# Performance work log

Measured on AMD Instinct MI355X. Metric: run time of the kernel, lower is better.

## Reference

```python
import jax, jax.numpy as jnp
import numpy as np

B, C, H, W = 4, 256, 64, 64

def _conv1x1(x, w, b):
    # x: (B,C,H,W), w: (O,C), b: (O,)  -> (B,O,H,W)
    return jnp.einsum('oc,bchw->bohw', w, x) + b[None, :, None, None]

def setup_inputs() -> dict:
    key = jax.random.key(0)
    ks = jax.random.split(key, 8)
    s = 1.0 / np.sqrt(C)  # conv weight init scale
    return {
        'tgt': jax.random.normal(ks[0], (B, C, H, W), jnp.float32),
        'src': jax.random.normal(ks[1], (B, C, H, W), jnp.float32),
        'q_w': jax.random.normal(ks[2], (C, C), jnp.float32) * s,
        'q_b': jnp.zeros((C,), jnp.float32),
        'k_w': jax.random.normal(ks[3], (C, C), jnp.float32) * s,
        'k_b': jnp.zeros((C,), jnp.float32),
        'v_w': jax.random.normal(ks[4], (C, C), jnp.float32) * s,
        'v_b': jnp.zeros((C,), jnp.float32),
    }

def reference(tgt, src, q_w, q_b, k_w, k_b, v_w, v_b):
    # NOTE: tgt.shape == src.shape here, so the interpolate branch is skipped.
    b, c, h, w = src.shape
    # Faithful to torch: .view(B, -1, C) is a RAW reshape of (B,O,H,W)
    # channel-first memory, NOT a transpose to (B, HW, C) token layout.
    query = _conv1x1(tgt, q_w, q_b).reshape(b, -1, c)  # (B, N, C), N = O*H*W/C = H*W
    key   = _conv1x1(src, k_w, k_b).reshape(b, -1, c)
    value = _conv1x1(src, v_w, v_b).reshape(b, -1, c)
    attn = jnp.einsum('bnc,bmc->bnm', query, key)       # (B, N, N) - materialized as in source
    attn = jax.nn.softmax(attn, axis=-1)
    out = jnp.einsum('bnm,bmc->bnc', attn, value)       # (B, N, C)
    return out.reshape(b, c, h, w)
```

## Files before the change

### kernel.cpp

```cpp
#include <hip/hip_runtime.h>
#include <cmath>

#define B_ 4
#define C_ 256
#define P_ 4096
#define N_ 4096

typedef __bf16 bf16x8 __attribute__((ext_vector_type(8)));
typedef __bf16 bf16x4 __attribute__((ext_vector_type(4)));
typedef float  f32x4  __attribute__((ext_vector_type(4)));

__global__ __launch_bounds__(256) void proj_kernel(
    const float* __restrict__ X, const float* __restrict__ W,
    const float* __restrict__ bias,
    __bf16* __restrict__ Yh, __bf16* __restrict__ Yl)
{
    const int p0 = blockIdx.x * 64;
    const int o0 = blockIdx.y * 64;
    const int b  = blockIdx.z;

    const float* Xb = X + (size_t)b * C_ * P_;
    const size_t ybase = (size_t)b * C_ * P_;

    __shared__ float WsT[32][68];
    __shared__ float Xs[32][64];

    const int tid = threadIdx.x;
    const int tx = tid & 15, ty = tid >> 4;

    float acc[4][4] = {};

    for (int kk = 0; kk < C_; kk += 32) {
        __syncthreads();
        #pragma unroll
        for (int i = 0; i < 8; ++i) {
            int flat = tid + i * 256;
            int r = flat >> 5, c = flat & 31;
            WsT[c][r] = W[(o0 + r) * C_ + (kk + c)];
        }
        #pragma unroll
        for (int i = 0; i < 8; ++i) {
            int flat = tid + i * 256;
            int r = flat >> 6, c = flat & 63;
            Xs[r][c] = Xb[(size_t)(kk + r) * P_ + (p0 + c)];
        }
        __syncthreads();
        #pragma unroll
        for (int k = 0; k < 32; ++k) {
            float4 a4 = *(const float4*)&WsT[k][ty * 4];
            float4 x4 = *(const float4*)&Xs[k][tx * 4];
            const float av[4] = {a4.x, a4.y, a4.z, a4.w};
            const float xv[4] = {x4.x, x4.y, x4.z, x4.w};
            #pragma unroll
            for (int i = 0; i < 4; ++i)
                #pragma unroll
                for (int j = 0; j < 4; ++j)
                    acc[i][j] += av[i] * xv[j];
        }
    }

    #pragma unroll
    for (int i = 0; i < 4; ++i) {
        float bv = bias[o0 + ty * 4 + i];
        bf16x4 h, l;
        #pragma unroll
        for (int j = 0; j < 4; ++j) {
            float y  = acc[i][j] + bv;
            __bf16 hh = (__bf16)y;
            __bf16 ll = (__bf16)(y - (float)hh);
            h[j] = hh; l[j] = ll;
        }
        size_t off = ybase + (size_t)(o0 + ty * 4 + i) * P_ + p0 + tx * 4;
        *(bf16x4*)&Yh[off] = h;
        *(bf16x4*)&Yl[off] = l;
    }
}

__global__ __launch_bounds__(256) void transpose_kernel(
    const ushort* __restrict__ Src, ushort* __restrict__ Dst)
{
    const int n0 = blockIdx.x * 64;
    const int c0 = blockIdx.y * 64;
    const int b  = blockIdx.z;

    const ushort* src = Src + (size_t)b * N_ * C_;
    ushort*       dst = Dst + (size_t)b * N_ * C_;

    __shared__ ushort T[64][65];
    const int tid = threadIdx.x;

    #pragma unroll
    for (int it = 0; it < 4; ++it) {
        int e = tid + it * 256;
        int r = e >> 4, c4 = (e & 15) * 4;
        *(ushort4*)&T[r][c4] = *(const ushort4*)&src[(size_t)(n0 + r) * C_ + c0 + c4];
    }
    __syncthreads();
    #pragma unroll
    for (int it = 0; it < 4; ++it) {
        int e = tid + it * 256;
        int cr = e >> 4, nl = (e & 15) * 4;
        ushort4 v;
        v.x = T[nl + 0][cr]; v.y = T[nl + 1][cr];
        v.z = T[nl + 2][cr]; v.w = T[nl + 3][cr];
        *(ushort4*)&dst[(size_t)(c0 + cr) * N_ + n0 + nl] = v;
    }
}

__global__ __launch_bounds__(256, 1) void attn_kernel(
    const __bf16* __restrict__ Qh, const __bf16* __restrict__ Ql,
    const __bf16* __restrict__ Kh, const __bf16* __restrict__ Kl,
    const __bf16* __restrict__ Vth,
    float* __restrict__ O)
{
    const int b  = blockIdx.y;
    const int n0 = blockIdx.x * 64;
    const size_t base = (size_t)b * N_ * C_;

    const int tid  = threadIdx.x;
    const int w    = tid >> 6;
    const int lane = tid & 63;
    const int l15  = lane & 15;
    const int lg   = lane >> 4;
    const int hsw  = l15 & 7;

    __shared__ __align__(16) __bf16 Ksh[2][64][256];
    __shared__ __align__(16) __bf16 Vsh[256][64];
    __shared__ __align__(16) __bf16 Pl[4][2][16][72];

    const __bf16* qh_p = Qh + base + (size_t)(n0 + w * 16 + l15) * C_ + lg * 8;
    const __bf16* ql_p = Ql + base + (size_t)(n0 + w * 16 + l15) * C_ + lg * 8;
    bf16x8 qfh[8], qfl[8];
    #pragma unroll
    for (int k = 0; k < 8; ++k) {
        qfh[k] = *(const bf16x8*)(qh_p + k * 32);
        qfl[k] = *(const bf16x8*)(ql_p + k * 32);
    }

    f32x4 oc[16];
    #pragma unroll
    for (int c = 0; c < 16; ++c) oc[c] = (f32x4){0.f, 0.f, 0.f, 0.f};
    float m_run[4] = {-1e30f, -1e30f, -1e30f, -1e30f};
    float l_run[4] = {0.f, 0.f, 0.f, 0.f};

    bf16x8 krH[8], krL[8], vrH[8];

    #pragma unroll
    for (int i = 0; i < 8; ++i) {
        int f = i * 256 + tid;
        int r = f >> 5, s = f & 31;
        krH[i] = *(const bf16x8*)(Kh + base + (size_t)(0 + r) * C_ + s * 8);
        krL[i] = *(const bf16x8*)(Kl + base + (size_t)(0 + r) * C_ + s * 8);
        int c = f >> 3, sv = f & 7;
        vrH[i] = *(const bf16x8*)(Vth + base + (size_t)c * N_ + 0 + sv * 8);
    }

    for (int mt = 0; mt < N_; mt += 64) {
        __syncthreads();

        #pragma unroll
        for (int i = 0; i < 8; ++i) {
            int f = i * 256 + tid;
            int r = f >> 5, s = f & 31;
            *(bf16x8*)&Ksh[0][r][(s ^ (r & 7)) * 8] = krH[i];
            *(bf16x8*)&Ksh[1][r][(s ^ (r & 7)) * 8] = krL[i];
            int c = f >> 3, sv = f & 7;
            *(bf16x8*)&Vsh[c][(sv ^ (c & 7)) * 8] = vrH[i];
        }
        __syncthreads();

        if (mt + 64 < N_) {
            const int nmt = mt + 64;
            #pragma unroll
            for (int i = 0; i < 8; ++i) {
                int f = i * 256 + tid;
                int r = f >> 5, s = f & 31;
                krH[i] = *(const bf16x8*)(Kh + base + (size_t)(nmt + r) * C_ + s * 8);
                krL[i] = *(const bf16x8*)(Kl + base + (size_t)(nmt + r) * C_ + s * 8);
                int c = f >> 3, sv = f & 7;
                vrH[i] = *(const bf16x8*)(Vth + base + (size_t)c * N_ + nmt + sv * 8);
            }
        }

        f32x4 sacc[4];
        #pragma unroll
        for (int js = 0; js < 4; ++js) sacc[js] = (f32x4){0.f, 0.f, 0.f, 0.f};

        #pragma unroll
        for (int kk = 0; kk < 8; ++kk) {
            #pragma unroll
            for (int js = 0; js < 4; ++js) {
                bf16x8 kfh = *(const bf16x8*)&Ksh[0][js * 16 + l15][((kk * 4 + lg) ^ hsw) * 8];
                bf16x8 kfl = *(const bf16x8*)&Ksh[1][js * 16 + l15][((kk * 4 + lg) ^ hsw) * 8];
                sacc[js] = __builtin_amdgcn_mfma_f32_16x16x32_bf16(qfh[kk], kfh, sacc[js], 0, 0, 0);
                sacc[js] = __builtin_amdgcn_mfma_f32_16x16x32_bf16(qfh[kk], kfl, sacc[js], 0, 0, 0);
                sacc[js] = __builtin_amdgcn_mfma_f32_16x16x32_bf16(qfl[kk], kfh, sacc[js], 0, 0, 0);
            }
        }

        #pragma unroll
        for (int r = 0; r < 4; ++r) {
            float mx = fmaxf(fmaxf(sacc[0][r], sacc[1][r]), fmaxf(sacc[2][r], sacc[3][r]));
            #pragma unroll
            for (int d = 1; d < 16; d <<= 1)
                mx = fmaxf(mx, __shfl_xor(mx, d, 64));
            if (mx > m_run[r]) {
                float scale = __expf(m_run[r] - mx);
                l_run[r] *= scale;
                #pragma unroll
                for (int c = 0; c < 16; ++c) oc[c][r] *= scale;
                m_run[r] = mx;
            }
            float ss = 0.f;
            #pragma unroll
            for (int js = 0; js < 4; ++js) {
                float pv = __expf(sacc[js][r] - m_run[r]);
                sacc[js][r] = pv;
                ss += pv;
            }
            #pragma unroll
            for (int d = 1; d < 16; d <<= 1)
                ss += __shfl_xor(ss, d, 64);
            l_run[r] += ss;
        }

        #pragma unroll
        for (int js = 0; js < 4; ++js)
            #pragma unroll
            for (int r = 0; r < 4; ++r) {
                float pv = sacc[js][r];
                __bf16 hh = (__bf16)pv;
                __bf16 ll = (__bf16)(pv - (float)hh);
                Pl[w][0][lg * 4 + r][js * 16 + l15] = hh;
                Pl[w][1][lg * 4 + r][js * 16 + l15] = ll;
            }

        bf16x8 pah0 = *(const bf16x8*)&Pl[w][0][l15][lg * 8];
        bf16x8 pah1 = *(const bf16x8*)&Pl[w][0][l15][32 + lg * 8];
        bf16x8 pal0 = *(const bf16x8*)&Pl[w][1][l15][lg * 8];
        bf16x8 pal1 = *(const bf16x8*)&Pl[w][1][l15][32 + lg * 8];

        #pragma unroll
        for (int cs = 0; cs < 16; ++cs) {
            bf16x8 vh0 = *(const bf16x8*)&Vsh[cs * 16 + l15][(lg ^ hsw) * 8];
            bf16x8 vh1 = *(const bf16x8*)&Vsh[cs * 16 + l15][((lg + 4) ^ hsw) * 8];
            f32x4 a = oc[cs];
            a = __builtin_amdgcn_mfma_f32_16x16x32_bf16(pah0, vh0, a, 0, 0, 0);
            a = __builtin_amdgcn_mfma_f32_16x16x32_bf16(pal0, vh0, a, 0, 0, 0);
            a = __builtin_amdgcn_mfma_f32_16x16x32_bf16(pah1, vh1, a, 0, 0, 0);
            a = __builtin_amdgcn_mfma_f32_16x16x32_bf16(pal1, vh1, a, 0, 0, 0);
            oc[cs] = a;
        }
    }

    float inv[4];
    #pragma unroll
    for (int r = 0; r < 4; ++r) inv[r] = 1.0f / l_run[r];
    #pragma unroll
    for (int cs = 0; cs < 16; ++cs)
        #pragma unroll
        for (int r = 0; r < 4; ++r)
            O[base + (size_t)(n0 + w * 16 + lg * 4 + r) * C_ + cs * 16 + l15] =
                oc[cs][r] * inv[r];
}

extern "C" void kernel_launch(void* const* d_in, const int* in_sizes, int n_in,
                              void* d_out, int out_size, void* d_ws, size_t ws_size,
                              hipStream_t stream)
{
    const float* tgt = (const float*)d_in[0];
    const float* src = (const float*)d_in[1];
    const float* qw  = (const float*)d_in[2];
    const float* qb  = (const float*)d_in[3];
    const float* kw  = (const float*)d_in[4];
    const float* kb  = (const float*)d_in[5];
    const float* vw  = (const float*)d_in[6];
    const float* vb  = (const float*)d_in[7];
    float* out = (float*)d_out;

    const size_t SZ = (size_t)B_ * N_ * C_;
    __bf16* w0 = (__bf16*)d_ws;
    __bf16* w1 = w0 + SZ;
    __bf16* w2 = w1 + SZ;
    __bf16* w3 = w2 + SZ;
    __bf16* w4 = w3 + SZ;

    dim3 pgrid(P_ / 64, C_ / 64, B_);
    proj_kernel<<<pgrid, 256, 0, stream>>>(src, vw, vb, w0, w1);
    dim3 tgrid(N_ / 64, C_ / 64, B_);
    transpose_kernel<<<tgrid, 256, 0, stream>>>((const ushort*)w0, (ushort*)w4);
    proj_kernel<<<pgrid, 256, 0, stream>>>(tgt, qw, qb, w0, w1);
    proj_kernel<<<pgrid, 256, 0, stream>>>(src, kw, kb, w2, w3);
    dim3 agrid(N_ / 64, B_);
    attn_kernel<<<agrid, 256, 0, stream>>>(w0, w1, w2, w3, w4, out);
}
```

Measured before the change: 557.7 us.

## Halve KV tile to 32 rows and target two blocks per CU

```diff
diff --git a/kernel.cpp b/kernel.cpp
--- a/kernel.cpp
+++ b/kernel.cpp
@@ -5,6 +5,7 @@
 #define C_ 256
 #define P_ 4096
 #define N_ 4096
+#define KVBLK 32
 
 typedef __bf16 bf16x8 __attribute__((ext_vector_type(8)));
 typedef __bf16 bf16x4 __attribute__((ext_vector_type(4)));
@@ -107,7 +108,7 @@
     }
 }
 
-__global__ __launch_bounds__(256, 1) void attn_kernel(
+__global__ __launch_bounds__(256, 2) void attn_kernel(
     const __bf16* __restrict__ Qh, const __bf16* __restrict__ Ql,
     const __bf16* __restrict__ Kh, const __bf16* __restrict__ Kl,
     const __bf16* __restrict__ Vth,
@@ -124,9 +125,9 @@
     const int lg   = lane >> 4;
     const int hsw  = l15 & 7;
 
-    __shared__ __align__(16) __bf16 Ksh[2][64][256];
-    __shared__ __align__(16) __bf16 Vsh[256][64];
-    __shared__ __align__(16) __bf16 Pl[4][2][16][72];
+    __shared__ __align__(16) __bf16 Ksh[2][KVBLK][256];
+    __shared__ __align__(16) __bf16 Vsh[256][40];
+    __shared__ __align__(16) __bf16 Pl[4][2][16][40];
 
     const __bf16* qh_p = Qh + base + (size_t)(n0 + w * 16 + l15) * C_ + lg * 8;
     const __bf16* ql_p = Ql + base + (size_t)(n0 + w * 16 + l15) * C_ + lg * 8;
@@ -143,53 +144,53 @@
     float m_run[4] = {-1e30f, -1e30f, -1e30f, -1e30f};
     float l_run[4] = {0.f, 0.f, 0.f, 0.f};
 
-    bf16x8 krH[8], krL[8], vrH[8];
-
-    #pragma unroll
-    for (int i = 0; i < 8; ++i) {
+    bf16x8 krH[4], krL[4], vrH[4];
+
+    #pragma unroll
+    for (int i = 0; i < 4; ++i) {
         int f = i * 256 + tid;
         int r = f >> 5, s = f & 31;
-        krH[i] = *(const bf16x8*)(Kh + base + (size_t)(0 + r) * C_ + s * 8);
-        krL[i] = *(const bf16x8*)(Kl + base + (size_t)(0 + r) * C_ + s * 8);
-        int c = f >> 3, sv = f & 7;
-        vrH[i] = *(const bf16x8*)(Vth + base + (size_t)c * N_ + 0 + sv * 8);
-    }
-
-    for (int mt = 0; mt < N_; mt += 64) {
-        __syncthreads();
-
-        #pragma unroll
-        for (int i = 0; i < 8; ++i) {
+        krH[i] = *(const bf16x8*)(Kh + base + (size_t)r * C_ + s * 8);
+        krL[i] = *(const bf16x8*)(Kl + base + (size_t)r * C_ + s * 8);
+        int c = f >> 2, sv = f & 3;
+        vrH[i] = *(const bf16x8*)(Vth + base + (size_t)c * N_ + sv * 8);
+    }
+
+    for (int mt = 0; mt < N_; mt += KVBLK) {
+        __syncthreads();
+
+        #pragma unroll
+        for (int i = 0; i < 4; ++i) {
             int f = i * 256 + tid;
             int r = f >> 5, s = f & 31;
             *(bf16x8*)&Ksh[0][r][(s ^ (r & 7)) * 8] = krH[i];
             *(bf16x8*)&Ksh[1][r][(s ^ (r & 7)) * 8] = krL[i];
-            int c = f >> 3, sv = f & 7;
-            *(bf16x8*)&Vsh[c][(sv ^ (c & 7)) * 8] = vrH[i];
-        }
-        __syncthreads();
-
-        if (mt + 64 < N_) {
-            const int nmt = mt + 64;
-            #pragma unroll
-            for (int i = 0; i < 8; ++i) {
+            int c = f >> 2, sv = f & 3;
+            *(bf16x8*)&Vsh[c][sv * 8] = vrH[i];
+        }
+        __syncthreads();
+
+        if (mt + KVBLK < N_) {
+            const int nmt = mt + KVBLK;
+            #pragma unroll
+            for (int i = 0; i < 4; ++i) {
                 int f = i * 256 + tid;
                 int r = f >> 5, s = f & 31;
                 krH[i] = *(const bf16x8*)(Kh + base + (size_t)(nmt + r) * C_ + s * 8);
                 krL[i] = *(const bf16x8*)(Kl + base + (size_t)(nmt + r) * C_ + s * 8);
-                int c = f >> 3, sv = f & 7;
+                int c = f >> 2, sv = f & 3;
                 vrH[i] = *(const bf16x8*)(Vth + base + (size_t)c * N_ + nmt + sv * 8);
             }
         }
 
-        f32x4 sacc[4];
-        #pragma unroll
-        for (int js = 0; js < 4; ++js) sacc[js] = (f32x4){0.f, 0.f, 0.f, 0.f};
+        f32x4 sacc[2];
+        #pragma unroll
+        for (int js = 0; js < 2; ++js) sacc[js] = (f32x4){0.f, 0.f, 0.f, 0.f};
 
         #pragma unroll
         for (int kk = 0; kk < 8; ++kk) {
             #pragma unroll
-            for (int js = 0; js < 4; ++js) {
+            for (int js = 0; js < 2; ++js) {
                 bf16x8 kfh = *(const bf16x8*)&Ksh[0][js * 16 + l15][((kk * 4 + lg) ^ hsw) * 8];
                 bf16x8 kfl = *(const bf16x8*)&Ksh[1][js * 16 + l15][((kk * 4 + lg) ^ hsw) * 8];
                 sacc[js] = __builtin_amdgcn_mfma_f32_16x16x32_bf16(qfh[kk], kfh, sacc[js], 0, 0, 0);
@@ -200,7 +201,7 @@
 
         #pragma unroll
         for (int r = 0; r < 4; ++r) {
-            float mx = fmaxf(fmaxf(sacc[0][r], sacc[1][r]), fmaxf(sacc[2][r], sacc[3][r]));
+            float mx = fmaxf(sacc[0][r], sacc[1][r]);
             #pragma unroll
             for (int d = 1; d < 16; d <<= 1)
                 mx = fmaxf(mx, __shfl_xor(mx, d, 64));
@@ -213,7 +214,7 @@
             }
             float ss = 0.f;
             #pragma unroll
-            for (int js = 0; js < 4; ++js) {
+            for (int js = 0; js < 2; ++js) {
                 float pv = __expf(sacc[js][r] - m_run[r]);
                 sacc[js][r] = pv;
                 ss += pv;
@@ -225,7 +226,7 @@
         }
 
         #pragma unroll
-        for (int js = 0; js < 4; ++js)
+        for (int js = 0; js < 2; ++js)
             #pragma unroll
             for (int r = 0; r < 4; ++r) {
                 float pv = sacc[js][r];
@@ -235,20 +236,15 @@
                 Pl[w][1][lg * 4 + r][js * 16 + l15] = ll;
             }
 
-        bf16x8 pah0 = *(const bf16x8*)&Pl[w][0][l15][lg * 8];
-        bf16x8 pah1 = *(const bf16x8*)&Pl[w][0][l15][32 + lg * 8];
-        bf16x8 pal0 = *(const bf16x8*)&Pl[w][1][l15][lg * 8];
-        bf16x8 pal1 = *(const bf16x8*)&Pl[w][1][l15][32 + lg * 8];
+        bf16x8 pah = *(const bf16x8*)&Pl[w][0][l15][lg * 8];
+        bf16x8 pal = *(const bf16x8*)&Pl[w][1][l15][lg * 8];
 
         #pragma unroll
         for (int cs = 0; cs < 16; ++cs) {
-            bf16x8 vh0 = *(const bf16x8*)&Vsh[cs * 16 + l15][(lg ^ hsw) * 8];
-            bf16x8 vh1 = *(const bf16x8*)&Vsh[cs * 16 + l15][((lg + 4) ^ hsw) * 8];
+            bf16x8 vh0 = *(const bf16x8*)&Vsh[cs * 16 + l15][lg * 8];
             f32x4 a = oc[cs];
-            a = __builtin_amdgcn_mfma_f32_16x16x32_bf16(pah0, vh0, a, 0, 0, 0);
-            a = __builtin_amdgcn_mfma_f32_16x16x32_bf16(pal0, vh0, a, 0, 0, 0);
-            a = __builtin_amdgcn_mfma_f32_16x16x32_bf16(pah1, vh1, a, 0, 0, 0);
-            a = __builtin_amdgcn_mfma_f32_16x16x32_bf16(pal1, vh1, a, 0, 0, 0);
+            a = __builtin_amdgcn_mfma_f32_16x16x32_bf16(pah, vh0, a, 0, 0, 0);
+            a = __builtin_amdgcn_mfma_f32_16x16x32_bf16(pal, vh0, a, 0, 0, 0);
             oc[cs] = a;
         }
     }
```

Measured after the change: 573.8 us. +2.9%, slower.
